# Kernel tuning notes

Hardware: AMD Instinct MI355X
Metric: run time of the kernel (lower is better)

The kernel has to match this reference:

```python
import jax, jax.numpy as jnp
import numpy as np

N_NODES = 50000
N_EDGES = 640000
HID = 128
IN_DIM = 3
N_LAYERS = 4


def _silu(x):
    return x * jax.nn.sigmoid(x)


def setup_inputs() -> dict:
    key = jax.random.key(0)
    ks = jax.random.split(key, 20)
    s = 0.05
    inp = {
        'nodes': jax.random.normal(ks[0], (N_NODES, IN_DIM), jnp.float32),
        'edges': jax.random.randint(ks[1], (2, N_EDGES), 0, N_NODES, jnp.int32),
        'edge_attr': jax.random.normal(ks[2], (N_EDGES, 1), jnp.float32),
        # embedding: Linear(input_dim, hidden)
        'emb_w': jax.random.normal(ks[3], (IN_DIM, HID), jnp.float32) * s,
        'emb_b': jnp.zeros((HID,), jnp.float32),
        # per-layer GCL params (stacked over layers)
        # edge_mlp: Linear(2*HID + 1, HID) -> SiLU -> Linear(HID, HID) -> SiLU
        'edge_w1': jax.random.normal(ks[4], (N_LAYERS, 2 * HID + 1, HID), jnp.float32) * s,
        'edge_b1': jnp.zeros((N_LAYERS, HID), jnp.float32),
        'edge_w2': jax.random.normal(ks[5], (N_LAYERS, HID, HID), jnp.float32) * s,
        'edge_b2': jnp.zeros((N_LAYERS, HID), jnp.float32),
        # node_mlp: Linear(2*HID, HID) -> SiLU -> Linear(HID, HID)
        'node_w1': jax.random.normal(ks[6], (N_LAYERS, 2 * HID, HID), jnp.float32) * s,
        'node_b1': jnp.zeros((N_LAYERS, HID), jnp.float32),
        'node_w2': jax.random.normal(ks[7], (N_LAYERS, HID, HID), jnp.float32) * s,
        'node_b2': jnp.zeros((N_LAYERS, HID), jnp.float32),
        # decoder: Linear(HID, HID) -> SiLU -> Linear(HID, 3)
        'dec_w1': jax.random.normal(ks[8], (HID, HID), jnp.float32) * s,
        'dec_b1': jnp.zeros((HID,), jnp.float32),
        'dec_w2': jax.random.normal(ks[9], (HID, 3), jnp.float32) * s,
        'dec_b2': jnp.zeros((3,), jnp.float32),
    }
    return inp


def reference(nodes, edges, edge_attr, emb_w, emb_b,
              edge_w1, edge_b1, edge_w2, edge_b2,
              node_w1, node_b1, node_w2, node_b2,
              dec_w1, dec_b1, dec_w2, dec_b2):
    row, col = edges[0], edges[1]
    n = nodes.shape[0]
    h = nodes @ emb_w + emb_b  # [N, HID]
    for l in range(N_LAYERS):
        # edge model: gather endpoints, MLP on [h_src, h_tgt, edge_attr]
        e_in = jnp.concatenate([h[row], h[col], edge_attr], axis=1)  # [E, 2H+1]
        m = _silu(e_in @ edge_w1[l] + edge_b1[l])
        m = _silu(m @ edge_w2[l] + edge_b2[l])  # [E, HID]
        # node model: scatter-sum messages to source nodes, then MLP
        agg = jax.ops.segment_sum(m, row, num_segments=n)  # [N, HID]
        u = jnp.concatenate([h, agg], axis=1)
        u = _silu(u @ node_w1[l] + node_b1[l])
        h = u @ node_w2[l] + node_b2[l]  # recurrent=False: no residual
    out = _silu(h @ dec_w1 + dec_b1)
    return out @ dec_w2 + dec_b2  # [N, 3]
```

## Files before the change

kernel.cpp:

```cpp
#include <hip/hip_runtime.h>

#define N_NODES 50000
#define N_EDGES 640000
#define HID 128
#define N_LAYERS 4
#define TILE_E 128

typedef _Float16 f16x8 __attribute__((ext_vector_type(8)));
typedef float f32x16 __attribute__((ext_vector_type(16)));

__device__ __forceinline__ float silu_f(float x) {
    return x * __builtin_amdgcn_rcpf(1.0f + __expf(-x));
}

__device__ __forceinline__ f32x16 zero16() {
    f32x16 z;
#pragma unroll
    for (int i = 0; i < 16; ++i) z[i] = 0.f;
    return z;
}

__global__ void k_embed(const float* __restrict__ nodes, const float* __restrict__ ew,
                        const float* __restrict__ eb, float* __restrict__ h) {
    int idx = blockIdx.x * 256 + threadIdx.x;
    if (idx >= N_NODES * HID) return;
    int i = idx >> 7, c = idx & 127;
    float n0 = nodes[i * 3 + 0], n1 = nodes[i * 3 + 1], n2 = nodes[i * 3 + 2];
    h[idx] = n0 * ew[c] + n1 * ew[HID + c] + n2 * ew[2 * HID + c] + eb[c];
}

__global__ void k_hist(const int* __restrict__ row, int* __restrict__ deg) {
    int e = blockIdx.x * 256 + threadIdx.x;
    if (e < N_EDGES) atomicAdd(&deg[row[e]], 1);
}

__global__ __launch_bounds__(1024) void k_scan(const int* __restrict__ deg, int* __restrict__ off) {
    __shared__ int partial[1024];
    const int t = threadIdx.x;
    const int chunk = (N_NODES + 1023) / 1024;
    const int base = t * chunk;
    int s = 0;
    for (int i = 0; i < chunk; ++i) {
        int idx = base + i;
        if (idx < N_NODES) s += deg[idx];
    }
    partial[t] = s;
    __syncthreads();
    for (int o = 1; o < 1024; o <<= 1) {
        int v = (t >= o) ? partial[t - o] : 0;
        __syncthreads();
        partial[t] += v;
        __syncthreads();
    }
    int run = (t == 0) ? 0 : partial[t - 1];
    for (int i = 0; i < chunk; ++i) {
        int idx = base + i;
        if (idx < N_NODES) {
            off[idx] = run;
            run += deg[idx];
        }
    }
}

__global__ void k_scatter(const int* __restrict__ row, const int* __restrict__ col,
                          const float* __restrict__ ea, int* __restrict__ off,
                          int* __restrict__ row_s, int* __restrict__ col_s,
                          float* __restrict__ ea_s) {
    int e = blockIdx.x * 256 + threadIdx.x;
    if (e >= N_EDGES) return;
    int r = row[e];
    int pos = atomicAdd(&off[r], 1);
    row_s[pos] = r;
    col_s[pos] = col[e];
    ea_s[pos] = ea[e];
}

__global__ __launch_bounds__(256) void k_packW2(const float* __restrict__ W2all,
                                                _Float16* __restrict__ W2p) {
    const int layer = blockIdx.x;
    const float* W2 = W2all + (size_t)layer * 128 * 128;
    _Float16* out = W2p + (size_t)layer * 128 * 128;
    const int t = threadIdx.x;
    for (int fl = t; fl < 2048; fl += 256) {
        int blk = fl >> 6, lane = fl & 63;
        int cb = blk >> 3, kb = blk & 7;
        int colg = cb * 32 + (lane & 31);
        int kbase = kb * 16 + (lane >> 5) * 8;
        f16x8 v;
#pragma unroll
        for (int j = 0; j < 8; ++j)
            v[j] = (_Float16)W2[(size_t)(kbase + j) * 128 + colg];
        *(f16x8*)&out[(size_t)fl * 8] = v;
    }
}

__global__ __launch_bounds__(256) void k_packAll(
    const float* __restrict__ ew1, const float* __restrict__ nw1,
    const float* __restrict__ nw2, const float* __restrict__ dw1,
    _Float16* __restrict__ WpA, _Float16* __restrict__ WpB,
    _Float16* __restrict__ WpN1, _Float16* __restrict__ WpN2,
    _Float16* __restrict__ WpD1) {
    const int b = blockIdx.x;
    const float* W; _Float16* dst; int K16;
    if (b < 4)       { W = ew1 + (size_t)b * 257 * 128;              dst = WpA  + (size_t)b * 32768; K16 = 8; }
    else if (b < 8)  { int l = b - 4;  W = ew1 + (size_t)l * 257 * 128 + 128 * 128; dst = WpB + (size_t)l * 32768; K16 = 8; }
    else if (b < 12) { int l = b - 8;  W = nw1 + (size_t)l * 256 * 128; dst = WpN1 + (size_t)l * 65536; K16 = 16; }
    else if (b < 16) { int l = b - 12; W = nw2 + (size_t)l * 128 * 128; dst = WpN2 + (size_t)l * 32768; K16 = 8; }
    else             { W = dw1; dst = WpD1; K16 = 8; }
    for (int fl = threadIdx.x; fl < K16 * 256; fl += 256) {
        int lane = fl & 63, cb = (fl >> 6) & 3, ks = fl >> 8;
        int col = cb * 32 + (lane & 31);
        int kb = ks * 16 + (lane >> 5) * 8;
        f16x8 h8, l8;
#pragma unroll
        for (int j = 0; j < 8; ++j) {
            float wv = W[(size_t)(kb + j) * 128 + col];
            _Float16 hh = (_Float16)wv;
            h8[j] = hh;
            l8[j] = (_Float16)((wv - (float)hh) * 2048.0f);
        }
        *(f16x8*)&dst[((size_t)(0 * K16 + ks) * 4 + cb) * 512 + lane * 8] = h8;
        *(f16x8*)&dst[((size_t)(1 * K16 + ks) * 4 + cb) * 512 + lane * 8] = l8;
    }
}

__global__ __launch_bounds__(512) void k_gemm3(
    const float* __restrict__ X1, const float* __restrict__ X2,
    const _Float16* __restrict__ Wp0, const float* __restrict__ bias0, float* __restrict__ out0,
    const _Float16* __restrict__ Wp1, const float* __restrict__ bias1, float* __restrict__ out1,
    int M, int K16, int do_silu) {
    const int t = threadIdx.x, w = t >> 6, l = t & 63;
    const int lane31 = l & 31, hi = l >> 5;
    const bool dual = (Wp1 != nullptr);
    int rb, cb0, sel;
    if (dual) { rb = w & 1; sel = w >> 2; cb0 = ((w >> 1) & 1) * 2; }
    else      { rb = w & 3; sel = 0;      cb0 = (w >> 2) * 2; }
    const int mtile = dual ? 64 : 128;
    const int m0 = blockIdx.x * mtile;
    const _Float16* Wp = sel ? Wp1 : Wp0;
    const float* bias = sel ? bias1 : bias0;
    float* out = sel ? out1 : out0;

    int rowg = m0 + rb * 32 + lane31;
    if (rowg >= M) rowg = M - 1;
    const int koff = hi * 8;

    f32x16 aH0 = zero16(), aH1 = zero16(), aL0 = zero16(), aL1 = zero16();
    const f16x8* Wv = (const f16x8*)Wp;
#pragma unroll 4
    for (int ks = 0; ks < K16; ++ks) {
        const float* Xp = (X2 != nullptr && ks >= 8) ? X2 : X1;
        const float* px = &Xp[(size_t)rowg * 128 + (ks & 7) * 16 + koff];
        float xv[8];
        *(float4*)&xv[0] = *(const float4*)px;
        *(float4*)&xv[4] = *(const float4*)(px + 4);
        f16x8 xh, xl;
#pragma unroll
        for (int q = 0; q < 8; ++q) {
            _Float16 hh = (_Float16)xv[q];
            xh[q] = hh;
            xl[q] = (_Float16)((xv[q] - (float)hh) * 2048.0f);
        }
        f16x8 bh0 = Wv[((size_t)ks * 4 + cb0) * 64 + l];
        f16x8 bh1 = Wv[((size_t)ks * 4 + cb0 + 1) * 64 + l];
        f16x8 bl0 = Wv[((size_t)(K16 + ks) * 4 + cb0) * 64 + l];
        f16x8 bl1 = Wv[((size_t)(K16 + ks) * 4 + cb0 + 1) * 64 + l];
        aH0 = __builtin_amdgcn_mfma_f32_32x32x16_f16(xh, bh0, aH0, 0, 0, 0);
        aH1 = __builtin_amdgcn_mfma_f32_32x32x16_f16(xh, bh1, aH1, 0, 0, 0);
        aL0 = __builtin_amdgcn_mfma_f32_32x32x16_f16(xh, bl0, aL0, 0, 0, 0);
        aL0 = __builtin_amdgcn_mfma_f32_32x32x16_f16(xl, bh0, aL0, 0, 0, 0);
        aL1 = __builtin_amdgcn_mfma_f32_32x32x16_f16(xh, bl1, aL1, 0, 0, 0);
        aL1 = __builtin_amdgcn_mfma_f32_32x32x16_f16(xl, bh1, aL1, 0, 0, 0);
    }
    const float inv = 1.0f / 2048.0f;
#pragma unroll
    for (int c = 0; c < 2; ++c) {
        int col = (cb0 + c) * 32 + lane31;
        float bv = bias ? bias[col] : 0.f;
        const f32x16& aH = c ? aH1 : aH0;
        const f32x16& aL = c ? aL1 : aL0;
#pragma unroll
        for (int r = 0; r < 16; ++r) {
            int gr = m0 + rb * 32 + (r & 3) + 8 * (r >> 2) + 4 * hi;
            if (gr < M) {
                float v = aH[r] + aL[r] * inv + bv;
                out[(size_t)gr * 128 + col] = do_silu ? silu_f(v) : v;
            }
        }
    }
}

__global__ __launch_bounds__(512) void k_dec(
    const float* __restrict__ X, const _Float16* __restrict__ WpD,
    const float* __restrict__ db1, const float* __restrict__ dw2,
    const float* __restrict__ db2, float* __restrict__ out, int M) {
    __shared__ float u_lds[128 * 133];
    __shared__ float w2_lds[384];
    const int t = threadIdx.x, w = t >> 6, l = t & 63;
    const int lane31 = l & 31, hi = l >> 5;
    const int rb = w & 3, cb0 = (w >> 2) * 2;
    const int m0 = blockIdx.x * 128;
    if (t < 384) w2_lds[t] = dw2[t];

    int rowg = m0 + rb * 32 + lane31;
    if (rowg >= M) rowg = M - 1;
    const int koff = hi * 8;

    f32x16 aH0 = zero16(), aH1 = zero16(), aL0 = zero16(), aL1 = zero16();
    const f16x8* Wv = (const f16x8*)WpD;
#pragma unroll
    for (int ks = 0; ks < 8; ++ks) {
        const float* px = &X[(size_t)rowg * 128 + ks * 16 + koff];
        float xv[8];
        *(float4*)&xv[0] = *(const float4*)px;
        *(float4*)&xv[4] = *(const float4*)(px + 4);
        f16x8 xh, xl;
#pragma unroll
        for (int q = 0; q < 8; ++q) {
            _Float16 hh = (_Float16)xv[q];
            xh[q] = hh;
            xl[q] = (_Float16)((xv[q] - (float)hh) * 2048.0f);
        }
        f16x8 bh0 = Wv[((size_t)ks * 4 + cb0) * 64 + l];
        f16x8 bh1 = Wv[((size_t)ks * 4 + cb0 + 1) * 64 + l];
        f16x8 bl0 = Wv[((size_t)(8 + ks) * 4 + cb0) * 64 + l];
        f16x8 bl1 = Wv[((size_t)(8 + ks) * 4 + cb0 + 1) * 64 + l];
        aH0 = __builtin_amdgcn_mfma_f32_32x32x16_f16(xh, bh0, aH0, 0, 0, 0);
        aH1 = __builtin_amdgcn_mfma_f32_32x32x16_f16(xh, bh1, aH1, 0, 0, 0);
        aL0 = __builtin_amdgcn_mfma_f32_32x32x16_f16(xh, bl0, aL0, 0, 0, 0);
        aL0 = __builtin_amdgcn_mfma_f32_32x32x16_f16(xl, bh0, aL0, 0, 0, 0);
        aL1 = __builtin_amdgcn_mfma_f32_32x32x16_f16(xh, bl1, aL1, 0, 0, 0);
        aL1 = __builtin_amdgcn_mfma_f32_32x32x16_f16(xl, bh1, aL1, 0, 0, 0);
    }
    const float inv = 1.0f / 2048.0f;
#pragma unroll
    for (int c = 0; c < 2; ++c) {
        int col = (cb0 + c) * 32 + lane31;
        float bv = db1[col];
        const f32x16& aH = c ? aH1 : aH0;
        const f32x16& aL = c ? aL1 : aL0;
#pragma unroll
        for (int r = 0; r < 16; ++r) {
            int lr = rb * 32 + (r & 3) + 8 * (r >> 2) + 4 * hi;
            u_lds[lr * 133 + col] = silu_f(aH[r] + aL[r] * inv + bv);
        }
    }
    __syncthreads();
    if (t < 384) {
        int rowl = t & 127, j = t >> 7;
        int gm = m0 + rowl;
        if (gm < M) {
            float s = db2[j];
            for (int c = 0; c < 128; ++c)
                s += u_lds[rowl * 133 + c] * w2_lds[c * 3 + j];
            out[(size_t)gm * 3 + j] = s;
        }
    }
}

__global__ __launch_bounds__(512, 4) void k_edge4(
    const float* __restrict__ A, const float* __restrict__ Bm,
    const float* __restrict__ w1last, const float* __restrict__ b2,
    const _Float16* __restrict__ W2p, const int* __restrict__ row_s,
    const int* __restrict__ col_s, const float* __restrict__ ea_s,
    float* __restrict__ agg) {
    __shared__ __align__(16) _Float16 W2s[16384];
    __shared__ __align__(16) _Float16 m1f[TILE_E * 136];
    __shared__ int rows_sh[TILE_E];
    __shared__ int segs_sh[TILE_E + 2];
    __shared__ unsigned long long masks_sh[2];

    const int t = threadIdx.x;
    const int w = t >> 6, l = t & 63;
    const int lane31 = l & 31, hi = l >> 5;

    for (int i = t; i < 2048; i += 512)
        ((float4*)W2s)[i] = ((const float4*)W2p)[i];

    const int e_mine = (w >> 1) * 32 + lane31;
    const int kbase0 = (w & 1) * 64 + hi * 8;

    const int rb_g = w & 3;
    const int cb0 = (w >> 2) * 2, cb1 = cb0 + 1;
    const float b20 = b2[cb0 * 32 + lane31];
    const float b21 = b2[cb1 * 32 + lane31];

    const f16x8* m1v = (const f16x8*)m1f;
    const f16x8* w2v = (const f16x8*)W2s;
    _Float16* mo = m1f;

    const int n_tiles = N_EDGES / TILE_E;
    const int stride = gridDim.x;

    int r_pf = 0; float ea_pf = 0.f;
    float bpf[32];

    auto issue_pf = [&](int tile) {
        int eg = tile * TILE_E + e_mine;
        r_pf = row_s[eg];
        int c = col_s[eg];
        ea_pf = ea_s[eg];
        const float* Bp = Bm + (size_t)c * 128;
#pragma unroll
        for (int j = 0; j < 4; ++j) {
            int k0 = kbase0 + j * 16;
            *(float4*)&bpf[j * 8] = *(const float4*)&Bp[k0];
            *(float4*)&bpf[j * 8 + 4] = *(const float4*)&Bp[k0 + 4];
        }
    };

    int tile = blockIdx.x;
    if (tile < n_tiles) issue_pf(tile);

    for (; tile < n_tiles; tile += stride) {
        __syncthreads();

        {
            const int r = r_pf;
            const float eav = ea_pf;
            const float* Ap = A + (size_t)r * 128;
#pragma unroll
            for (int j = 0; j < 4; ++j) {
                int k0 = kbase0 + j * 16;
                float av[8], wv_[8];
                *(float4*)&av[0] = *(const float4*)&Ap[k0];
                *(float4*)&av[4] = *(const float4*)&Ap[k0 + 4];
                *(float4*)&wv_[0] = *(const float4*)&w1last[k0];
                *(float4*)&wv_[4] = *(const float4*)&w1last[k0 + 4];
                f16x8 o;
#pragma unroll
                for (int q = 0; q < 8; ++q)
                    o[q] = (_Float16)silu_f(av[q] + bpf[j * 8 + q] + eav * wv_[q]);
                *(f16x8*)&m1f[(w * 4 + j) * 512 + l * 8] = o;
            }
            if ((w & 1) == 0 && hi == 0) rows_sh[e_mine] = r;
        }
        __syncthreads();

        if (t < 128) {
            bool flag = (t == 0) || (rows_sh[t] != rows_sh[t - 1]);
            unsigned long long m = __ballot(flag);
            if ((t & 63) == 0) masks_sh[t >> 6] = m;
        }

        int nt = tile + stride;
        if (nt < n_tiles) issue_pf(nt);

        f32x16 acc0 = zero16(), acc1 = zero16();
#pragma unroll
        for (int kb = 0; kb < 8; ++kb) {
            f16x8 a = m1v[(rb_g * 8 + kb) * 64 + l];
            acc0 = __builtin_amdgcn_mfma_f32_32x32x16_f16(a, w2v[(cb0 * 8 + kb) * 64 + l], acc0, 0, 0, 0);
            acc1 = __builtin_amdgcn_mfma_f32_32x32x16_f16(a, w2v[(cb1 * 8 + kb) * 64 + l], acc1, 0, 0, 0);
        }
        __syncthreads();

        const unsigned long long m0 = masks_sh[0], m1m = masks_sh[1];
        const int ns = __popcll(m0) + __popcll(m1m);
        if (t < 128) {
            bool bit = (t < 64) ? ((m0 >> t) & 1ull) : ((m1m >> (t - 64)) & 1ull);
            if (bit) {
                int idx = (t < 64) ? __popcll(m0 & ((1ull << t) - 1))
                                   : __popcll(m0) + __popcll(m1m & ((1ull << (t - 64)) - 1));
                segs_sh[idx] = t;
            }
        }
        if (t == 0) segs_sh[ns] = TILE_E;

#pragma unroll
        for (int r = 0; r < 16; ++r) {
            int rowi = (r & 3) + 8 * (r >> 2) + 4 * hi;
            int erow = rb_g * 32 + rowi;
            mo[erow * 136 + cb0 * 32 + lane31] = (_Float16)silu_f(acc0[r] + b20);
            mo[erow * 136 + cb1 * 32 + lane31] = (_Float16)silu_f(acc1[r] + b21);
        }
        __syncthreads();

        {
            const int c = t & 127, g = t >> 7;
            for (int s = g; s < ns; s += 4) {
                int st = segs_sh[s], en = segs_sh[s + 1];
                float sum = 0.f;
                for (int q = st; q < en; ++q) sum += (float)mo[q * 136 + c];
                atomicAdd(&agg[(size_t)rows_sh[st] * 128 + c], sum);
            }
        }
    }
}

extern "C" void kernel_launch(void* const* d_in, const int* in_sizes, int n_in,
                              void* d_out, int out_size, void* d_ws, size_t ws_size,
                              hipStream_t stream) {
    const float* nodes = (const float*)d_in[0];
    const int* edges = (const int*)d_in[1];
    const float* ea = (const float*)d_in[2];
    const float* emb_w = (const float*)d_in[3];
    const float* emb_b = (const float*)d_in[4];
    const float* ew1 = (const float*)d_in[5];
    const float* eb1 = (const float*)d_in[6];
    const float* ew2 = (const float*)d_in[7];
    const float* eb2 = (const float*)d_in[8];
    const float* nw1 = (const float*)d_in[9];
    const float* nb1 = (const float*)d_in[10];
    const float* nw2 = (const float*)d_in[11];
    const float* nb2 = (const float*)d_in[12];
    const float* dw1 = (const float*)d_in[13];
    const float* db1 = (const float*)d_in[14];
    const float* dw2 = (const float*)d_in[15];
    const float* db2 = (const float*)d_in[16];
    const int* row = edges;
    const int* col = edges + N_EDGES;

    const size_t NH = (size_t)N_NODES * HID;
    float* r0 = (float*)d_ws;
    float* r1 = r0 + NH;
    float* r2 = r1 + NH;
    float* r3 = r2 + NH;
    int* deg = (int*)(r3 + NH);
    int* off = deg + N_NODES;
    int* row_s = off + N_NODES;
    int* col_s = row_s + N_EDGES;
    float* ea_s = (float*)(col_s + N_EDGES);
    _Float16* W2p = (_Float16*)(ea_s + N_EDGES);
    _Float16* WpA  = W2p  + (size_t)4 * 16384;
    _Float16* WpB  = WpA  + (size_t)4 * 32768;
    _Float16* WpN1 = WpB  + (size_t)4 * 32768;
    _Float16* WpN2 = WpN1 + (size_t)4 * 65536;
    _Float16* WpD1 = WpN2 + (size_t)4 * 32768;

    float* h = r0;
    float* other = r2;

    hipMemsetAsync(deg, 0, N_NODES * sizeof(int), stream);
    k_hist<<<(N_EDGES + 255) / 256, 256, 0, stream>>>(row, deg);
    k_scan<<<1, 1024, 0, stream>>>(deg, off);
    k_scatter<<<(N_EDGES + 255) / 256, 256, 0, stream>>>(row, col, ea, off, row_s, col_s, ea_s);
    k_packW2<<<N_LAYERS, 256, 0, stream>>>(ew2, W2p);
    k_packAll<<<17, 256, 0, stream>>>(ew1, nw1, nw2, dw1, WpA, WpB, WpN1, WpN2, WpD1);

    k_embed<<<(N_NODES * HID + 255) / 256, 256, 0, stream>>>(nodes, emb_w, emb_b, h);

    const int g128 = (N_NODES + 127) / 128;
    const int g64 = (N_NODES + 63) / 64;
    for (int l = 0; l < N_LAYERS; ++l) {
        const float* W1 = ew1 + (size_t)l * 257 * 128;
        k_gemm3<<<g64, 512, 0, stream>>>(h, nullptr,
                                         WpA + (size_t)l * 32768, eb1 + l * 128, r1,
                                         WpB + (size_t)l * 32768, nullptr, other,
                                         N_NODES, 8, 0);
        hipMemsetAsync(r3, 0, NH * sizeof(float), stream);
        k_edge4<<<512, 512, 0, stream>>>(r1, other, W1 + 256 * 128, eb2 + l * 128,
                                         W2p + (size_t)l * 128 * 128, row_s, col_s, ea_s, r3);
        k_gemm3<<<g128, 512, 0, stream>>>(h, r3,
                                          WpN1 + (size_t)l * 65536, nb1 + l * 128, r1,
                                          nullptr, nullptr, nullptr,
                                          N_NODES, 16, 1);
        k_gemm3<<<g128, 512, 0, stream>>>(r1, nullptr,
                                          WpN2 + (size_t)l * 32768, nb2 + l * 128, other,
                                          nullptr, nullptr, nullptr,
                                          N_NODES, 8, 0);
        float* tmp = h; h = other; other = tmp;
    }
    k_dec<<<g128, 512, 0, stream>>>(h, WpD1, db1, dw2, db2, (float*)d_out, N_NODES);
}
```

Before: 1.009 ms.

## Fuse node MLP with next-layer edge projections and decoder; slim edge kernel

Adds a k_node kernel that chains node_w1 (with SiLU), node_w2, and either the next layer's edge projections A/B or the decoder MLP, keeping intermediates in LDS so they skip round trips through global memory and separate launches. The edge kernel drops its LDS copy of W2 and reads W2 fragments straight from global memory. It also stops prefetching the gathered B rows and loads them at use time. Launch bounds and grid size change to allow more occupancy (8 blocks per CU, 1024 blocks). The risk is that W2 reads from global/L2 and unprefetched gathers stall the edge kernel, and k_node uses more LDS with lower parallelism per tile.

```diff
diff --git a/kernel.cpp b/kernel.cpp
--- a/kernel.cpp
+++ b/kernel.cpp
@@ -124,6 +124,15 @@
     }
 }
 
+__device__ __forceinline__ void split8(const float* xv, f16x8& xh, f16x8& xl) {
+#pragma unroll
+    for (int q = 0; q < 8; ++q) {
+        _Float16 hh = (_Float16)xv[q];
+        xh[q] = hh;
+        xl[q] = (_Float16)((xv[q] - (float)hh) * 2048.0f);
+    }
+}
+
 __global__ __launch_bounds__(512) void k_gemm3(
     const float* __restrict__ X1, const float* __restrict__ X2,
     const _Float16* __restrict__ Wp0, const float* __restrict__ bias0, float* __restrict__ out0,
@@ -155,12 +164,7 @@
         *(float4*)&xv[0] = *(const float4*)px;
         *(float4*)&xv[4] = *(const float4*)(px + 4);
         f16x8 xh, xl;
-#pragma unroll
-        for (int q = 0; q < 8; ++q) {
-            _Float16 hh = (_Float16)xv[q];
-            xh[q] = hh;
-            xl[q] = (_Float16)((xv[q] - (float)hh) * 2048.0f);
-        }
+        split8(xv, xh, xl);
         f16x8 bh0 = Wv[((size_t)ks * 4 + cb0) * 64 + l];
         f16x8 bh1 = Wv[((size_t)ks * 4 + cb0 + 1) * 64 + l];
         f16x8 bl0 = Wv[((size_t)(K16 + ks) * 4 + cb0) * 64 + l];
@@ -190,81 +194,206 @@
     }
 }
 
-__global__ __launch_bounds__(512) void k_dec(
-    const float* __restrict__ X, const _Float16* __restrict__ WpD,
-    const float* __restrict__ db1, const float* __restrict__ dw2,
-    const float* __restrict__ db2, float* __restrict__ out, int M) {
+__global__ __launch_bounds__(512, 4) void k_node(
+    float* __restrict__ h, const float* __restrict__ agg,
+    const _Float16* __restrict__ Wn1, const float* __restrict__ nb1,
+    const _Float16* __restrict__ Wn2, const float* __restrict__ nb2,
+    const _Float16* __restrict__ WA, const float* __restrict__ ebA,
+    const _Float16* __restrict__ WB,
+    float* __restrict__ outA, float* __restrict__ outB,
+    const _Float16* __restrict__ WD, const float* __restrict__ db1,
+    const float* __restrict__ dw2, const float* __restrict__ db2,
+    float* __restrict__ dec_out, int M, int final_mode) {
     __shared__ float u_lds[128 * 133];
-    __shared__ float w2_lds[384];
+    __shared__ float w2l[384];
     const int t = threadIdx.x, w = t >> 6, l = t & 63;
     const int lane31 = l & 31, hi = l >> 5;
     const int rb = w & 3, cb0 = (w >> 2) * 2;
     const int m0 = blockIdx.x * 128;
-    if (t < 384) w2_lds[t] = dw2[t];
+    const int koff = hi * 8;
+    const float inv = 1.0f / 2048.0f;
+
+    if (final_mode && t < 384) w2l[t] = dw2[t];
 
     int rowg = m0 + rb * 32 + lane31;
     if (rowg >= M) rowg = M - 1;
-    const int koff = hi * 8;
-
-    f32x16 aH0 = zero16(), aH1 = zero16(), aL0 = zero16(), aL1 = zero16();
-    const f16x8* Wv = (const f16x8*)WpD;
-#pragma unroll
-    for (int ks = 0; ks < 8; ++ks) {
-        const float* px = &X[(size_t)rowg * 128 + ks * 16 + koff];
-        float xv[8];
-        *(float4*)&xv[0] = *(const float4*)px;
-        *(float4*)&xv[4] = *(const float4*)(px + 4);
-        f16x8 xh, xl;
-#pragma unroll
-        for (int q = 0; q < 8; ++q) {
-            _Float16 hh = (_Float16)xv[q];
-            xh[q] = hh;
-            xl[q] = (_Float16)((xv[q] - (float)hh) * 2048.0f);
-        }
-        f16x8 bh0 = Wv[((size_t)ks * 4 + cb0) * 64 + l];
-        f16x8 bh1 = Wv[((size_t)ks * 4 + cb0 + 1) * 64 + l];
-        f16x8 bl0 = Wv[((size_t)(8 + ks) * 4 + cb0) * 64 + l];
-        f16x8 bl1 = Wv[((size_t)(8 + ks) * 4 + cb0 + 1) * 64 + l];
-        aH0 = __builtin_amdgcn_mfma_f32_32x32x16_f16(xh, bh0, aH0, 0, 0, 0);
-        aH1 = __builtin_amdgcn_mfma_f32_32x32x16_f16(xh, bh1, aH1, 0, 0, 0);
-        aL0 = __builtin_amdgcn_mfma_f32_32x32x16_f16(xh, bl0, aL0, 0, 0, 0);
-        aL0 = __builtin_amdgcn_mfma_f32_32x32x16_f16(xl, bh0, aL0, 0, 0, 0);
-        aL1 = __builtin_amdgcn_mfma_f32_32x32x16_f16(xh, bl1, aL1, 0, 0, 0);
-        aL1 = __builtin_amdgcn_mfma_f32_32x32x16_f16(xl, bh1, aL1, 0, 0, 0);
-    }
-    const float inv = 1.0f / 2048.0f;
-#pragma unroll
-    for (int c = 0; c < 2; ++c) {
-        int col = (cb0 + c) * 32 + lane31;
-        float bv = db1[col];
-        const f32x16& aH = c ? aH1 : aH0;
-        const f32x16& aL = c ? aL1 : aL0;
-#pragma unroll
-        for (int r = 0; r < 16; ++r) {
-            int lr = rb * 32 + (r & 3) + 8 * (r >> 2) + 4 * hi;
-            u_lds[lr * 133 + col] = silu_f(aH[r] + aL[r] * inv + bv);
+
+    {
+        f32x16 aH0 = zero16(), aH1 = zero16(), aL0 = zero16(), aL1 = zero16();
+        const f16x8* Wv = (const f16x8*)Wn1;
+#pragma unroll 4
+        for (int ks = 0; ks < 16; ++ks) {
+            const float* Xp = (ks >= 8) ? agg : h;
+            const float* px = &Xp[(size_t)rowg * 128 + (ks & 7) * 16 + koff];
+            float xv[8];
+            *(float4*)&xv[0] = *(const float4*)px;
+            *(float4*)&xv[4] = *(const float4*)(px + 4);
+            f16x8 xh, xl;
+            split8(xv, xh, xl);
+            f16x8 bh0 = Wv[((size_t)ks * 4 + cb0) * 64 + l];
+            f16x8 bh1 = Wv[((size_t)ks * 4 + cb0 + 1) * 64 + l];
+            f16x8 bl0 = Wv[((size_t)(16 + ks) * 4 + cb0) * 64 + l];
+            f16x8 bl1 = Wv[((size_t)(16 + ks) * 4 + cb0 + 1) * 64 + l];
+            aH0 = __builtin_amdgcn_mfma_f32_32x32x16_f16(xh, bh0, aH0, 0, 0, 0);
+            aH1 = __builtin_amdgcn_mfma_f32_32x32x16_f16(xh, bh1, aH1, 0, 0, 0);
+            aL0 = __builtin_amdgcn_mfma_f32_32x32x16_f16(xh, bl0, aL0, 0, 0, 0);
+            aL0 = __builtin_amdgcn_mfma_f32_32x32x16_f16(xl, bh0, aL0, 0, 0, 0);
+            aL1 = __builtin_amdgcn_mfma_f32_32x32x16_f16(xh, bl1, aL1, 0, 0, 0);
+            aL1 = __builtin_amdgcn_mfma_f32_32x32x16_f16(xl, bh1, aL1, 0, 0, 0);
+        }
+#pragma unroll
+        for (int c = 0; c < 2; ++c) {
+            int col = (cb0 + c) * 32 + lane31;
+            float bv = nb1[col];
+            const f32x16& aH = c ? aH1 : aH0;
+            const f32x16& aL = c ? aL1 : aL0;
+#pragma unroll
+            for (int r = 0; r < 16; ++r) {
+                int lr = rb * 32 + (r & 3) + 8 * (r >> 2) + 4 * hi;
+                u_lds[lr * 133 + col] = silu_f(aH[r] + aL[r] * inv + bv);
+            }
         }
     }
     __syncthreads();
-    if (t < 384) {
-        int rowl = t & 127, j = t >> 7;
-        int gm = m0 + rowl;
-        if (gm < M) {
-            float s = db2[j];
-            for (int c = 0; c < 128; ++c)
-                s += u_lds[rowl * 133 + c] * w2_lds[c * 3 + j];
-            out[(size_t)gm * 3 + j] = s;
-        }
-    }
-}
-
-__global__ __launch_bounds__(512, 4) void k_edge4(
+
+    {
+        f32x16 aH0 = zero16(), aH1 = zero16(), aL0 = zero16(), aL1 = zero16();
+        const f16x8* Wv = (const f16x8*)Wn2;
+#pragma unroll
+        for (int ks = 0; ks < 8; ++ks) {
+            float xv[8];
+            const int base = (rb * 32 + lane31) * 133 + ks * 16 + koff;
+#pragma unroll
+            for (int q = 0; q < 8; ++q) xv[q] = u_lds[base + q];
+            f16x8 xh, xl;
+            split8(xv, xh, xl);
+            f16x8 bh0 = Wv[((size_t)ks * 4 + cb0) * 64 + l];
+            f16x8 bh1 = Wv[((size_t)ks * 4 + cb0 + 1) * 64 + l];
+            f16x8 bl0 = Wv[((size_t)(8 + ks) * 4 + cb0) * 64 + l];
+            f16x8 bl1 = Wv[((size_t)(8 + ks) * 4 + cb0 + 1) * 64 + l];
+            aH0 = __builtin_amdgcn_mfma_f32_32x32x16_f16(xh, bh0, aH0, 0, 0, 0);
+            aH1 = __builtin_amdgcn_mfma_f32_32x32x16_f16(xh, bh1, aH1, 0, 0, 0);
+            aL0 = __builtin_amdgcn_mfma_f32_32x32x16_f16(xh, bl0, aL0, 0, 0, 0);
+            aL0 = __builtin_amdgcn_mfma_f32_32x32x16_f16(xl, bh0, aL0, 0, 0, 0);
+            aL1 = __builtin_amdgcn_mfma_f32_32x32x16_f16(xh, bl1, aL1, 0, 0, 0);
+            aL1 = __builtin_amdgcn_mfma_f32_32x32x16_f16(xl, bh1, aL1, 0, 0, 0);
+        }
+        __syncthreads();
+#pragma unroll
+        for (int c = 0; c < 2; ++c) {
+            int col = (cb0 + c) * 32 + lane31;
+            float bv = nb2[col];
+            const f32x16& aH = c ? aH1 : aH0;
+            const f32x16& aL = c ? aL1 : aL0;
+#pragma unroll
+            for (int r = 0; r < 16; ++r) {
+                int lr = rb * 32 + (r & 3) + 8 * (r >> 2) + 4 * hi;
+                float v = aH[r] + aL[r] * inv + bv;
+                u_lds[lr * 133 + col] = v;
+                int gr = m0 + lr;
+                if (!final_mode && gr < M) h[(size_t)gr * 128 + col] = v;
+            }
+        }
+    }
+    __syncthreads();
+
+    if (!final_mode) {
+#pragma unroll
+        for (int pass = 0; pass < 2; ++pass) {
+            const int sel = w >> 2, w2 = w & 3;
+            const int cbp = w2 >> 1, cb0p = (cbp) * 2;
+            const int rb3 = (w2 & 1) * 2 + pass;
+            const _Float16* Wp = sel ? WB : WA;
+            float* op = sel ? outB : outA;
+            f32x16 aH0 = zero16(), aH1 = zero16(), aL0 = zero16(), aL1 = zero16();
+            const f16x8* Wv = (const f16x8*)Wp;
+#pragma unroll
+            for (int ks = 0; ks < 8; ++ks) {
+                float xv[8];
+                const int base = (rb3 * 32 + lane31) * 133 + ks * 16 + koff;
+#pragma unroll
+                for (int q = 0; q < 8; ++q) xv[q] = u_lds[base + q];
+                f16x8 xh, xl;
+                split8(xv, xh, xl);
+                f16x8 bh0 = Wv[((size_t)ks * 4 + cb0p) * 64 + l];
+                f16x8 bh1 = Wv[((size_t)ks * 4 + cb0p + 1) * 64 + l];
+                f16x8 bl0 = Wv[((size_t)(8 + ks) * 4 + cb0p) * 64 + l];
+                f16x8 bl1 = Wv[((size_t)(8 + ks) * 4 + cb0p + 1) * 64 + l];
+                aH0 = __builtin_amdgcn_mfma_f32_32x32x16_f16(xh, bh0, aH0, 0, 0, 0);
+                aH1 = __builtin_amdgcn_mfma_f32_32x32x16_f16(xh, bh1, aH1, 0, 0, 0);
+                aL0 = __builtin_amdgcn_mfma_f32_32x32x16_f16(xh, bl0, aL0, 0, 0, 0);
+                aL0 = __builtin_amdgcn_mfma_f32_32x32x16_f16(xl, bh0, aL0, 0, 0, 0);
+                aL1 = __builtin_amdgcn_mfma_f32_32x32x16_f16(xh, bl1, aL1, 0, 0, 0);
+                aL1 = __builtin_amdgcn_mfma_f32_32x32x16_f16(xl, bh1, aL1, 0, 0, 0);
+            }
+#pragma unroll
+            for (int c = 0; c < 2; ++c) {
+                int col = (cb0p + c) * 32 + lane31;
+                float bv = sel ? 0.f : ebA[col];
+                const f32x16& aH = c ? aH1 : aH0;
+                const f32x16& aL = c ? aL1 : aL0;
+#pragma unroll
+                for (int r = 0; r < 16; ++r) {
+                    int gr = m0 + rb3 * 32 + (r & 3) + 8 * (r >> 2) + 4 * hi;
+                    if (gr < M) op[(size_t)gr * 128 + col] = aH[r] + aL[r] * inv + bv;
+                }
+            }
+        }
+    } else {
+        f32x16 aH0 = zero16(), aH1 = zero16(), aL0 = zero16(), aL1 = zero16();
+        const f16x8* Wv = (const f16x8*)WD;
+#pragma unroll
+        for (int ks = 0; ks < 8; ++ks) {
+            float xv[8];
+            const int base = (rb * 32 + lane31) * 133 + ks * 16 + koff;
+#pragma unroll
+            for (int q = 0; q < 8; ++q) xv[q] = u_lds[base + q];
+            f16x8 xh, xl;
+            split8(xv, xh, xl);
+            f16x8 bh0 = Wv[((size_t)ks * 4 + cb0) * 64 + l];
+            f16x8 bh1 = Wv[((size_t)ks * 4 + cb0 + 1) * 64 + l];
+            f16x8 bl0 = Wv[((size_t)(8 + ks) * 4 + cb0) * 64 + l];
+            f16x8 bl1 = Wv[((size_t)(8 + ks) * 4 + cb0 + 1) * 64 + l];
+            aH0 = __builtin_amdgcn_mfma_f32_32x32x16_f16(xh, bh0, aH0, 0, 0, 0);
+            aH1 = __builtin_amdgcn_mfma_f32_32x32x16_f16(xh, bh1, aH1, 0, 0, 0);
+            aL0 = __builtin_amdgcn_mfma_f32_32x32x16_f16(xh, bl0, aL0, 0, 0, 0);
+            aL0 = __builtin_amdgcn_mfma_f32_32x32x16_f16(xl, bh0, aL0, 0, 0, 0);
+            aL1 = __builtin_amdgcn_mfma_f32_32x32x16_f16(xh, bl1, aL1, 0, 0, 0);
+            aL1 = __builtin_amdgcn_mfma_f32_32x32x16_f16(xl, bh1, aL1, 0, 0, 0);
+        }
+        __syncthreads();
+#pragma unroll
+        for (int c = 0; c < 2; ++c) {
+            int col = (cb0 + c) * 32 + lane31;
+            float bv = db1[col];
+            const f32x16& aH = c ? aH1 : aH0;
+            const f32x16& aL = c ? aL1 : aL0;
+#pragma unroll
+            for (int r = 0; r < 16; ++r) {
+                int lr = rb * 32 + (r & 3) + 8 * (r >> 2) + 4 * hi;
+                u_lds[lr * 133 + col] = silu_f(aH[r] + aL[r] * inv + bv);
+            }
+        }
+        __syncthreads();
+        if (t < 384) {
+            int rowl = t & 127, j = t >> 7;
+            int gm = m0 + rowl;
+            if (gm < M) {
+                float s = db2[j];
+                for (int c = 0; c < 128; ++c)
+                    s += u_lds[rowl * 133 + c] * w2l[c * 3 + j];
+                dec_out[(size_t)gm * 3 + j] = s;
+            }
+        }
+    }
+}
+
+__global__ __launch_bounds__(512, 8) void k_edge5(
     const float* __restrict__ A, const float* __restrict__ Bm,
     const float* __restrict__ w1last, const float* __restrict__ b2,
     const _Float16* __restrict__ W2p, const int* __restrict__ row_s,
     const int* __restrict__ col_s, const float* __restrict__ ea_s,
     float* __restrict__ agg) {
-    __shared__ __align__(16) _Float16 W2s[16384];
     __shared__ __align__(16) _Float16 m1f[TILE_E * 136];
     __shared__ int rows_sh[TILE_E];
     __shared__ int segs_sh[TILE_E + 2];
@@ -274,9 +403,6 @@
     const int w = t >> 6, l = t & 63;
     const int lane31 = l & 31, hi = l >> 5;
 
-    for (int i = t; i < 2048; i += 512)
-        ((float4*)W2s)[i] = ((const float4*)W2p)[i];
-
     const int e_mine = (w >> 1) * 32 + lane31;
     const int kbase0 = (w & 1) * 64 + hi * 8;
 
@@ -286,27 +412,18 @@
     const float b21 = b2[cb1 * 32 + lane31];
 
     const f16x8* m1v = (const f16x8*)m1f;
-    const f16x8* w2v = (const f16x8*)W2s;
+    const f16x8* w2v = (const f16x8*)W2p;
     _Float16* mo = m1f;
 
     const int n_tiles = N_EDGES / TILE_E;
     const int stride = gridDim.x;
 
-    int r_pf = 0; float ea_pf = 0.f;
-    float bpf[32];
-
+    int r_pf = 0, c_pf = 0; float ea_pf = 0.f;
     auto issue_pf = [&](int tile) {
         int eg = tile * TILE_E + e_mine;
         r_pf = row_s[eg];
-        int c = col_s[eg];
+        c_pf = col_s[eg];
         ea_pf = ea_s[eg];
-        const float* Bp = Bm + (size_t)c * 128;
-#pragma unroll
-        for (int j = 0; j < 4; ++j) {
-            int k0 = kbase0 + j * 16;
-            *(float4*)&bpf[j * 8] = *(const float4*)&Bp[k0];
-            *(float4*)&bpf[j * 8 + 4] = *(const float4*)&Bp[k0 + 4];
-        }
     };
 
     int tile = blockIdx.x;
@@ -319,21 +436,24 @@
             const int r = r_pf;
             const float eav = ea_pf;
             const float* Ap = A + (size_t)r * 128;
+            const float* Bp = Bm + (size_t)c_pf * 128;
 #pragma unroll
             for (int j = 0; j < 4; ++j) {
                 int k0 = kbase0 + j * 16;
-                float av[8], wv_[8];
+                float av[8], bv[8], wv_[8];
                 *(float4*)&av[0] = *(const float4*)&Ap[k0];
                 *(float4*)&av[4] = *(const float4*)&Ap[k0 + 4];
+                *(float4*)&bv[0] = *(const float4*)&Bp[k0];
+                *(float4*)&bv[4] = *(const float4*)&Bp[k0 + 4];
                 *(float4*)&wv_[0] = *(const float4*)&w1last[k0];
                 *(float4*)&wv_[4] = *(const float4*)&w1last[k0 + 4];
                 f16x8 o;
 #pragma unroll
                 for (int q = 0; q < 8; ++q)
-                    o[q] = (_Float16)silu_f(av[q] + bpf[j * 8 + q] + eav * wv_[q]);
+                    o[q] = (_Float16)silu_f(av[q] + bv[q] + eav * wv_[q]);
                 *(f16x8*)&m1f[(w * 4 + j) * 512 + l * 8] = o;
             }
-            if ((w & 1) == 0 && hi == 0) rows_sh[e_mine] = r;
+            if ((w & 1) == 0 && hi == 0) rows_sh[e_mine] = r_pf;
         }
         __syncthreads();
 
@@ -428,9 +548,6 @@
     _Float16* WpN2 = WpN1 + (size_t)4 * 65536;
     _Float16* WpD1 = WpN2 + (size_t)4 * 32768;
 
-    float* h = r0;
-    float* other = r2;
-
     hipMemsetAsync(deg, 0, N_NODES * sizeof(int), stream);
     k_hist<<<(N_EDGES + 255) / 256, 256, 0, stream>>>(row, deg);
     k_scan<<<1, 1024, 0, stream>>>(deg, off);
@@ -438,28 +555,40 @@
     k_packW2<<<N_LAYERS, 256, 0, stream>>>(ew2, W2p);
     k_packAll<<<17, 256, 0, stream>>>(ew1, nw1, nw2, dw1, WpA, WpB, WpN1, WpN2, WpD1);
 
-    k_embed<<<(N_NODES * HID + 255) / 256, 256, 0, stream>>>(nodes, emb_w, emb_b, h);
-
+    k_embed<<<(N_NODES * HID + 255) / 256, 256, 0, stream>>>(nodes, emb_w, emb_b, r0);
+
+    const int g64 = (N_NODES + 63) / 64;
     const int g128 = (N_NODES + 127) / 128;
-    const int g64 = (N_NODES + 63) / 64;
+
+    k_gemm3<<<g64, 512, 0, stream>>>(r0, nullptr,
+                                     WpA, eb1, r1,
+                                     WpB, nullptr, r2,
+                                     N_NODES, 8, 0);
+
     for (int l = 0; l < N_LAYERS; ++l) {
-        const float* W1 = ew1 + (size_t)l * 257 * 128;
-        k_gemm3<<<g64, 512, 0, stream>>>(h, nullptr,
-                                         WpA + (size_t)l * 32768, eb1 + l * 128, r1,
-                                         WpB + (size_t)l * 32768, nullptr, other,
-                                         N_NODES, 8, 0);
         hipMemsetAsync(r3, 0, NH * sizeof(float), stream);
-        k_edge4<<<512, 512, 0, stream>>>(r1, other, W1 + 256 * 128, eb2 + l * 128,
-                                         W2p + (size_t)l * 128 * 128, row_s, col_s, ea_s, r3);
-        k_gemm3<<<g128, 512, 0, stream>>>(h, r3,
-                                          WpN1 + (size_t)l * 65536, nb1 + l * 128, r1,
-                                          nullptr, nullptr, nullptr,
-                                          N_NODES, 16, 1);
-        k_gemm3<<<g128, 512, 0, stream>>>(r1, nullptr,
-                                          WpN2 + (size_t)l * 32768, nb2 + l * 128, other,
-                                          nullptr, nullptr, nullptr,
-                                          N_NODES, 8, 0);
-        float* tmp = h; h = other; other = tmp;
-    }
-    k_dec<<<g128, 512, 0, stream>>>(h, WpD1, db1, dw2, db2, (float*)d_out, N_NODES);
-}
+        k_edge5<<<1024, 512, 0, stream>>>(r1, r2,
+                                          ew1 + (size_t)l * 257 * 128 + 256 * 128,
+                                          eb2 + l * 128,
+                                          W2p + (size_t)l * 16384,
+                                          row_s, col_s, ea_s, r3);
+        if (l < N_LAYERS - 1) {
+            k_node<<<g128, 512, 0, stream>>>(r0, r3,
+                                             WpN1 + (size_t)l * 65536, nb1 + l * 128,
+                                             WpN2 + (size_t)l * 32768, nb2 + l * 128,
+                                             WpA + (size_t)(l + 1) * 32768, eb1 + (l + 1) * 128,
+                                             WpB + (size_t)(l + 1) * 32768,
+                                             r1, r2,
+                                             nullptr, nullptr, nullptr, nullptr, nullptr,
+                                             N_NODES, 0);
+        } else {
+            k_node<<<g128, 512, 0, stream>>>(r0, r3,
+                                             WpN1 + (size_t)l * 65536, nb1 + l * 128,
+                                             WpN2 + (size_t)l * 32768, nb2 + l * 128,
+                                             nullptr, nullptr, nullptr,
+                                             nullptr, nullptr,
+                                             WpD1, db1, dw2, db2,
+                                             (float*)d_out, N_NODES, 1);
+        }
+    }
+}
```

Result: slower. 1.618 ms (+60.3%).
